# Optimization experiments

Hardware: AMD Instinct MI355X
Metric: run time of the kernel (lower is better)

## Reference

```python
import jax, jax.numpy as jnp
import numpy as np

N_HEADS = 16
PROJ_DIM = 64  # per-head dim
DIM = N_HEADS * PROJ_DIM  # 1024


def setup_inputs() -> dict:
    key = jax.random.key(0)
    k1, k2, k3, k4, k5 = jax.random.split(key, 5)
    N, L = 2, 2048
    scale = 1.0 / np.sqrt(DIM)
    return {
        "query": jax.random.normal(k1, (N, L, DIM), dtype=jnp.float32),
        "key": jax.random.normal(k2, (N, L, DIM), dtype=jnp.float32),
        "Wq": jax.random.normal(k3, (DIM, DIM), dtype=jnp.float32) * scale,
        "Wk": jax.random.normal(k4, (DIM, DIM), dtype=jnp.float32) * scale,
        "Wv": jax.random.normal(k5, (DIM, DIM), dtype=jnp.float32) * scale,
    }


def reference(query, key, Wq, Wk, Wv):
    # Causal linear-complexity attention (mask=True branch, left_first=False).
    N, Lq, _ = query.shape
    Lk = key.shape[1]
    H, Dh = N_HEADS, PROJ_DIM
    # torch Linear: x @ W.T ; reshape to (N, H, L, Dh)
    q = (query @ Wq.T).reshape(N, Lq, H, Dh).transpose(0, 2, 1, 3)
    k = (key @ Wk.T).reshape(N, Lk, H, Dh).transpose(0, 2, 1, 3)
    v = (key @ Wv.T).reshape(N, Lk, H, Dh).transpose(0, 2, 1, 3)
    q = jax.nn.softmax(q, axis=-1)
    k = jax.nn.softmax(k, axis=-1)
    # right[t] = sum_{s<=t} k_s^T v_s  : (N,H,Lk,Dh,Dh) cumulative outer products
    S = jnp.cumsum(jnp.einsum('nhti,nhtj->nhtij', k, v), axis=2)
    out = jnp.einsum('nhti,nhtij->nhtj', q, S)  # (N,H,Lq,Dh)
    return out.transpose(0, 2, 1, 3).reshape(N, Lq, H * Dh)
```

## Files before the change

kernel.cpp:

```cpp
#include <hip/hip_runtime.h>


constexpr int DIM  = 1024;
constexpr int H    = 16;
constexpr int DH   = 64;
constexpr int LSEQ = 2048;
constexpr int NB   = 2;
constexpr int MTOK = NB * LSEQ;
constexpr int CS   = 64;
constexpr int NC   = LSEQ / CS;

typedef __bf16 bf16x8 __attribute__((ext_vector_type(8)));
typedef float floatx4 __attribute__((ext_vector_type(4)));
typedef unsigned short ushort_t;

__device__ __forceinline__ ushort_t f2bf(float f) {
  unsigned int u = __float_as_uint(f);
  u += 0x7FFFu + ((u >> 16) & 1u);
  return (ushort_t)(u >> 16);
}
__device__ __forceinline__ float bf2f(ushort_t b) {
  return __uint_as_float(((unsigned int)b) << 16);
}

__device__ __forceinline__ void async16(void* lds, const void* g) {
  __builtin_amdgcn_global_load_lds(
      (const __attribute__((address_space(1))) unsigned int*)g,
      (__attribute__((address_space(3))) unsigned int*)lds, 16, 0, 0);
}

__device__ __forceinline__ bf16x8 tfrag(const unsigned int* T, int row, int uoff) {
  union { bf16x8 v; unsigned int u[4]; } r;
  const unsigned int* p = T + row * 33 + uoff;
  r.u[0] = p[0]; r.u[1] = p[1]; r.u[2] = p[2]; r.u[3] = p[3];
  return r.v;
}

__device__ __forceinline__ void transpose_tile(const ushort_t* g, unsigned int* TT, int tid) {
  const int ic = tid & 7, tp = tid >> 3;
  const ushort_t* r0 = g + (size_t)(2 * tp) * DIM + ic * 8;
  union { uint4 q; ushort_t u[8]; } a0, a1;
  a0.q = *(const uint4*)r0;
  a1.q = *(const uint4*)(r0 + DIM);
#pragma unroll
  for (int j = 0; j < 8; j++)
    TT[(8 * ic + j) * 33 + tp] = (unsigned int)a0.u[j] | ((unsigned int)a1.u[j] << 16);
}

__global__ __launch_bounds__(256) void cast_all(const float* __restrict__ q,
                                                const float* __restrict__ k,
                                                const float* __restrict__ wq,
                                                const float* __restrict__ wk,
                                                const float* __restrict__ wv,
                                                ushort_t* __restrict__ xbf,
                                                ushort_t* __restrict__ wbf) {
  const int seg = blockIdx.y;
  const float* src;
  ushort_t* dst;
  int n4;
  if (seg == 0)      { src = q;  dst = xbf;                  n4 = (4 << 20) / 4; }
  else if (seg == 1) { src = k;  dst = xbf + (4 << 20);      n4 = (4 << 20) / 4; }
  else if (seg == 2) { src = wq; dst = wbf;                  n4 = (1 << 20) / 4; }
  else if (seg == 3) { src = wk; dst = wbf + (1 << 20);      n4 = (1 << 20) / 4; }
  else               { src = wv; dst = wbf + (2 << 20);      n4 = (1 << 20) / 4; }
  for (int i = blockIdx.x * 256 + threadIdx.x; i < n4; i += gridDim.x * 256) {
    const float4 f = ((const float4*)src)[i];
    ((ushort4*)dst)[i] = make_ushort4(f2bf(f.x), f2bf(f.y), f2bf(f.z), f2bf(f.w));
  }
}

struct Stage { ushort_t As[128 * 32]; ushort_t Ws[128 * 32]; };
union SMemU { Stage st[3]; ushort_t CsB[128 * 136]; };

__global__ __launch_bounds__(256) void gemm_fused(const ushort_t* __restrict__ xbf,
                                                  const ushort_t* __restrict__ wbf,
                                                  ushort_t* __restrict__ qp,
                                                  ushort_t* __restrict__ kp,
                                                  ushort_t* __restrict__ vp) {
  __shared__ SMemU sm;
  const int tid  = threadIdx.x;
  const int z    = blockIdx.z;
  const ushort_t* A = xbf + (z ? (size_t)(4 << 20) : 0);
  const ushort_t* W = wbf + (size_t)z * (1 << 20);
  ushort_t* C = (z == 0) ? qp : ((z == 1) ? kp : vp);
  const int bn   = blockIdx.x * 128;
  const int bm   = blockIdx.y * 128;
  const int lane = tid & 63;
  const int wid  = tid >> 6;
  const int wm   = wid >> 1, wn = wid & 1;
  const int row16 = lane & 15, quad = lane >> 4;

  floatx4 acc[4][4] = {};

  const int srow = tid >> 2;
  const int cg   = (tid & 3) ^ ((srow ^ (srow >> 2)) & 3);
  const ushort_t* gA0 = A + (size_t)(bm + srow) * DIM + cg * 8;
  const ushort_t* gA1 = A + (size_t)(bm + 64 + srow) * DIM + cg * 8;
  const ushort_t* gW0 = W + (size_t)(bn + srow) * DIM + cg * 8;
  const ushort_t* gW1 = W + (size_t)(bn + 64 + srow) * DIM + cg * 8;

#define STAGE(buf, koff)                                    \
  {                                                         \
    Stage& s_ = sm.st[buf];                                 \
    async16(s_.As + tid * 8,         gA0 + (koff));         \
    async16(s_.As + (tid + 256) * 8, gA1 + (koff));         \
    async16(s_.Ws + tid * 8,         gW0 + (koff));         \
    async16(s_.Ws + (tid + 256) * 8, gW1 + (koff));         \
  }

  const int qx   = quad ^ ((row16 ^ (row16 >> 2)) & 3);
  const int aoff = (wm * 64 + row16) * 32 + qx * 8;
  const int boff = (wn * 64 + row16) * 32 + qx * 8;

  STAGE(0, 0);
  STAGE(1, 32);

  int cur = 0, pf = 2;
  for (int s = 0; s < 32; ++s) {
    if (s < 31) asm volatile("s_waitcnt vmcnt(4)" ::: "memory");
    else        asm volatile("s_waitcnt vmcnt(0)" ::: "memory");
    __builtin_amdgcn_s_barrier();
    if (s + 2 < 32) STAGE(pf, (s + 2) * 32);

    const Stage& st = sm.st[cur];
    bf16x8 a[4], b[4];
#pragma unroll
    for (int mt = 0; mt < 4; mt++)
      a[mt] = *(const bf16x8*)&st.As[aoff + mt * 512];
#pragma unroll
    for (int nt = 0; nt < 4; nt++)
      b[nt] = *(const bf16x8*)&st.Ws[boff + nt * 512];
#pragma unroll
    for (int mt = 0; mt < 4; mt++)
#pragma unroll
      for (int nt = 0; nt < 4; nt++)
        acc[mt][nt] = __builtin_amdgcn_mfma_f32_16x16x32_bf16(a[mt], b[nt], acc[mt][nt], 0, 0, 0);

    cur = (cur == 2) ? 0 : cur + 1;
    pf  = (pf  == 2) ? 0 : pf + 1;
  }
#undef STAGE
  __syncthreads();

  if (z < 2) {
#pragma unroll
    for (int mt = 0; mt < 4; mt++)
#pragma unroll
      for (int r = 0; r < 4; r++) {
        float m = fmaxf(fmaxf(acc[mt][0][r], acc[mt][1][r]),
                        fmaxf(acc[mt][2][r], acc[mt][3][r]));
#pragma unroll
        for (int o = 1; o < 16; o <<= 1) m = fmaxf(m, __shfl_xor(m, o, 64));
        float e[4], s = 0.f;
#pragma unroll
        for (int nt = 0; nt < 4; nt++) { e[nt] = __expf(acc[mt][nt][r] - m); s += e[nt]; }
#pragma unroll
        for (int o = 1; o < 16; o <<= 1) s += __shfl_xor(s, o, 64);
        const float inv = 1.f / s;
#pragma unroll
        for (int nt = 0; nt < 4; nt++) acc[mt][nt][r] = e[nt] * inv;
      }
  }

#pragma unroll
  for (int mt = 0; mt < 4; mt++)
#pragma unroll
    for (int nt = 0; nt < 4; nt++)
#pragma unroll
      for (int r = 0; r < 4; r++)
        sm.CsB[(wm * 64 + mt * 16 + quad * 4 + r) * 136 + wn * 64 + nt * 16 + row16] =
            f2bf(acc[mt][nt][r]);
  __syncthreads();
#pragma unroll
  for (int it = 0; it < 8; it++) {
    const int ch = tid + it * 256;
    const int row = ch >> 4, ic = ch & 15;
    const uint4 val = *(const uint4*)&sm.CsB[row * 136 + ic * 8];
    *(uint4*)&C[(size_t)(bm + row) * DIM + bn + ic * 8] = val;
  }
}

__global__ __launch_bounds__(256) void chunk_T(const ushort_t* __restrict__ kp,
                                               const ushort_t* __restrict__ vp,
                                               float* __restrict__ cs) {
  __shared__ unsigned int KT[64 * 33];
  __shared__ unsigned int VT[64 * 33];
  const int c = blockIdx.x, h = blockIdx.y, n = blockIdx.z;
  const int tid = threadIdx.x;
  const size_t gbase = ((size_t)(n * LSEQ + c * CS)) * DIM + h * DH;

  transpose_tile(kp + gbase, KT, tid);
  transpose_tile(vp + gbase, VT, tid);
  __syncthreads();

  const int lane = tid & 63, wid = tid >> 6;
  const int row16 = lane & 15, quad = lane >> 4;

  floatx4 acc[4] = {};
#pragma unroll
  for (int ks = 0; ks < 2; ks++) {
    const bf16x8 a = tfrag(VT, wid * 16 + row16, ks * 16 + quad * 4);
#pragma unroll
    for (int nt = 0; nt < 4; nt++) {
      const bf16x8 b = tfrag(KT, nt * 16 + row16, ks * 16 + quad * 4);
      acc[nt] = __builtin_amdgcn_mfma_f32_16x16x32_bf16(a, b, acc[nt], 0, 0, 0);
    }
  }
  float* outp = cs + ((size_t)((n * H + h) * NC + c)) * (DH * DH);
#pragma unroll
  for (int nt = 0; nt < 4; nt++)
#pragma unroll
    for (int r = 0; r < 4; r++)
      outp[(wid * 16 + quad * 4 + r) * DH + nt * 16 + row16] = acc[nt][r];
}

__global__ __launch_bounds__(256) void prefix_chunks(const float* __restrict__ cs,
                                                     ushort_t* __restrict__ csb) {
  const int nh = blockIdx.x >> 4;
  const int e  = (blockIdx.x & 15) * 256 + threadIdx.x;
  const float* bf_ = cs + (size_t)nh * NC * (DH * DH) + e;
  ushort_t* bb = csb + (size_t)nh * NC * (DH * DH) + e;
  float run = 0.f;
#pragma unroll
  for (int c = 0; c < NC; c++) {
    const float cur = bf_[(size_t)c * (DH * DH)];
    bb[(size_t)c * (DH * DH)] = f2bf(run);
    run += cur;
  }
}

__global__ __launch_bounds__(256) void attn_mfma(const ushort_t* __restrict__ qp,
                                                 const ushort_t* __restrict__ kp,
                                                 const ushort_t* __restrict__ vp,
                                                 const ushort_t* __restrict__ csb,
                                                 float* __restrict__ out) {
  __shared__ ushort_t Qs[64 * 72];
  __shared__ ushort_t Ks[64 * 72];
  __shared__ ushort_t Ts[64 * 72];
  __shared__ unsigned int VT[64 * 33];
  __shared__ ushort_t Pb[64 * 72];
  const int c = blockIdx.x, h = blockIdx.y, n = blockIdx.z;
  const int tid = threadIdx.x;
  const size_t gbase = ((size_t)(n * LSEQ + c * CS)) * DIM + h * DH;
  const size_t cbase = ((size_t)((n * H + h) * NC + c)) * (DH * DH);

#pragma unroll
  for (int it = 0; it < 2; it++) {
    const int ch = tid + it * 256;
    const int row = ch >> 3, ic = ch & 7;
    *(uint4*)&Qs[row * 72 + ic * 8] = *(const uint4*)&qp[gbase + (size_t)row * DIM + ic * 8];
    *(uint4*)&Ks[row * 72 + ic * 8] = *(const uint4*)&kp[gbase + (size_t)row * DIM + ic * 8];
    *(uint4*)&Ts[row * 72 + ic * 8] = *(const uint4*)&csb[cbase + (size_t)row * DH + ic * 8];
  }
  transpose_tile(vp + gbase, VT, tid);
  __syncthreads();

  const int lane = tid & 63, wid = tid >> 6;
  const int row16 = lane & 15, quad = lane >> 4;
  const int t0 = wid * 16;

  floatx4 acc[4] = {};
  floatx4 pacc[4] = {};

#pragma unroll
  for (int ks = 0; ks < 2; ks++) {
    const bf16x8 aq = *(const bf16x8*)&Qs[(t0 + row16) * 72 + ks * 32 + quad * 8];
#pragma unroll
    for (int nt = 0; nt < 4; nt++) {
      const bf16x8 bt = *(const bf16x8*)&Ts[(nt * 16 + row16) * 72 + ks * 32 + quad * 8];
      acc[nt] = __builtin_amdgcn_mfma_f32_16x16x32_bf16(aq, bt, acc[nt], 0, 0, 0);
      const bf16x8 bk = *(const bf16x8*)&Ks[(nt * 16 + row16) * 72 + ks * 32 + quad * 8];
      pacc[nt] = __builtin_amdgcn_mfma_f32_16x16x32_bf16(aq, bk, pacc[nt], 0, 0, 0);
    }
  }
#pragma unroll
  for (int nt = 0; nt < 4; nt++)
#pragma unroll
    for (int r = 0; r < 4; r++) {
      const int t = t0 + quad * 4 + r, s = nt * 16 + row16;
      Pb[t * 72 + s] = f2bf((s <= t) ? pacc[nt][r] : 0.f);
    }
  __syncthreads();

#pragma unroll
  for (int ks = 0; ks < 2; ks++) {
    const bf16x8 ap = *(const bf16x8*)&Pb[(t0 + row16) * 72 + ks * 32 + quad * 8];
#pragma unroll
    for (int nt = 0; nt < 4; nt++) {
      const bf16x8 bv = tfrag(VT, nt * 16 + row16, ks * 16 + quad * 4);
      acc[nt] = __builtin_amdgcn_mfma_f32_16x16x32_bf16(ap, bv, acc[nt], 0, 0, 0);
    }
  }

#pragma unroll
  for (int nt = 0; nt < 4; nt++)
#pragma unroll
    for (int r = 0; r < 4; r++)
      out[gbase + (size_t)(t0 + quad * 4 + r) * DIM + nt * 16 + row16] = acc[nt][r];
}

extern "C" void kernel_launch(void* const* d_in, const int* in_sizes, int n_in,
                              void* d_out, int out_size, void* d_ws, size_t ws_size,
                              hipStream_t stream) {
  const float* query = (const float*)d_in[0];
  const float* key   = (const float*)d_in[1];
  const float* Wq    = (const float*)d_in[2];
  const float* Wk    = (const float*)d_in[3];
  const float* Wv    = (const float*)d_in[4];
  float* out = (float*)d_out;

  const size_t PM = (size_t)4 << 20;
  ushort_t* qp = (ushort_t*)d_ws;
  ushort_t* kp = qp + PM;
  ushort_t* vp = kp + PM;
  float*    cs = (float*)(vp + PM);
  ushort_t* csb = (ushort_t*)(cs + PM);
  ushort_t* xbf = (ushort_t*)cs;
  ushort_t* wbf = (ushort_t*)out;

  cast_all<<<dim3(512, 5), 256, 0, stream>>>(query, key, Wq, Wk, Wv, xbf, wbf);

  gemm_fused<<<dim3(DIM / 128, MTOK / 128, 3), 256, 0, stream>>>(xbf, wbf, qp, kp, vp);

  chunk_T<<<dim3(NC, H, NB), 256, 0, stream>>>(kp, vp, cs);
  prefix_chunks<<<dim3(NB * H * 16), 256, 0, stream>>>(cs, csb);
  attn_mfma<<<dim3(NC, H, NB), 256, 0, stream>>>(qp, kp, vp, csb, out);
}
```

Baseline: 158.2 us.

## Fuse chunk, prefix and attention stages into persistent kernel with grid barriers

Replaces the three tail launches (per-chunk KᵀV, chunk prefix sum, per-chunk attention) with one persistent 768-block kernel. Each block handles one or two tiles, and the stages are separated by a software grid barrier built on global atomics. Separately, the projection GEMM moves to a flat 1D grid with an XCD-aware remap, so blocks sharing the same A rows land on the same XCD's L2. This removes launch gaps and improves cache locality. It depends on all 768 blocks being co-resident; if they are not, the spin barrier can deadlock.

```diff
diff --git a/kernel.cpp b/kernel.cpp
--- a/kernel.cpp
+++ b/kernel.cpp
@@ -9,6 +9,8 @@
 constexpr int MTOK = NB * LSEQ;
 constexpr int CS   = 64;
 constexpr int NC   = LSEQ / CS;
+constexpr int NTILE = NC * H * NB;
+constexpr int TGRID = 768;
 
 typedef __bf16 bf16x8 __attribute__((ext_vector_type(8)));
 typedef float floatx4 __attribute__((ext_vector_type(4)));
@@ -18,9 +20,6 @@
   unsigned int u = __float_as_uint(f);
   u += 0x7FFFu + ((u >> 16) & 1u);
   return (ushort_t)(u >> 16);
-}
-__device__ __forceinline__ float bf2f(ushort_t b) {
-  return __uint_as_float(((unsigned int)b) << 16);
 }
 
 __device__ __forceinline__ void async16(void* lds, const void* g) {
@@ -45,6 +44,27 @@
 #pragma unroll
   for (int j = 0; j < 8; j++)
     TT[(8 * ic + j) * 33 + tp] = (unsigned int)a0.u[j] | ((unsigned int)a1.u[j] << 16);
+}
+
+__device__ int g_bar = 0;
+__device__ int g_gen = 0;
+
+__device__ __forceinline__ void grid_sync_all() {
+  __syncthreads();
+  if (threadIdx.x == 0) {
+    __threadfence();
+    const int g = __hip_atomic_load(&g_gen, __ATOMIC_RELAXED, __HIP_MEMORY_SCOPE_AGENT);
+    if (__hip_atomic_fetch_add(&g_bar, 1, __ATOMIC_ACQ_REL, __HIP_MEMORY_SCOPE_AGENT)
+        == TGRID - 1) {
+      __hip_atomic_store(&g_bar, 0, __ATOMIC_RELAXED, __HIP_MEMORY_SCOPE_AGENT);
+      __hip_atomic_fetch_add(&g_gen, 1, __ATOMIC_RELEASE, __HIP_MEMORY_SCOPE_AGENT);
+    } else {
+      while (__hip_atomic_load(&g_gen, __ATOMIC_ACQUIRE, __HIP_MEMORY_SCOPE_AGENT) == g)
+        __builtin_amdgcn_s_sleep(1);
+    }
+    __threadfence();
+  }
+  __syncthreads();
 }
 
 __global__ __launch_bounds__(256) void cast_all(const float* __restrict__ q,
@@ -79,12 +99,18 @@
                                                   ushort_t* __restrict__ vp) {
   __shared__ SMemU sm;
   const int tid  = threadIdx.x;
-  const int z    = blockIdx.z;
+
+  const int flat  = blockIdx.x;
+  const int xcd   = flat & 7;
+  const int local = flat >> 3;
+  const int z     = local >> 5;
+  const int l2    = local & 31;
+  const int bn    = (l2 & 7) * 128;
+  const int bm    = (xcd * 4 + (l2 >> 3)) * 128;
+
   const ushort_t* A = xbf + (z ? (size_t)(4 << 20) : 0);
   const ushort_t* W = wbf + (size_t)z * (1 << 20);
   ushort_t* C = (z == 0) ? qp : ((z == 1) ? kp : vp);
-  const int bn   = blockIdx.x * 128;
-  const int bm   = blockIdx.y * 128;
   const int lane = tid & 63;
   const int wid  = tid >> 6;
   const int wm   = wid >> 1, wn = wid & 1;
@@ -180,123 +206,130 @@
   }
 }
 
-__global__ __launch_bounds__(256) void chunk_T(const ushort_t* __restrict__ kp,
-                                               const ushort_t* __restrict__ vp,
-                                               float* __restrict__ cs) {
-  __shared__ unsigned int KT[64 * 33];
+__global__ __launch_bounds__(256, 3) void fused_tail(const ushort_t* __restrict__ qp,
+                                                     const ushort_t* __restrict__ kp,
+                                                     const ushort_t* __restrict__ vp,
+                                                     float* __restrict__ cs,
+                                                     ushort_t* __restrict__ csb,
+                                                     float* __restrict__ out) {
   __shared__ unsigned int VT[64 * 33];
-  const int c = blockIdx.x, h = blockIdx.y, n = blockIdx.z;
+  __shared__ union TailU {
+    unsigned int KT[64 * 33];
+    struct { ushort_t Qs[64 * 72]; ushort_t Ks[64 * 72];
+             ushort_t Ts[64 * 72]; ushort_t Pb[64 * 72]; } p3;
+  } u;
+
+  const int blk = blockIdx.x;
   const int tid = threadIdx.x;
-  const size_t gbase = ((size_t)(n * LSEQ + c * CS)) * DIM + h * DH;
-
-  transpose_tile(kp + gbase, KT, tid);
-  transpose_tile(vp + gbase, VT, tid);
-  __syncthreads();
-
   const int lane = tid & 63, wid = tid >> 6;
   const int row16 = lane & 15, quad = lane >> 4;
 
-  floatx4 acc[4] = {};
-#pragma unroll
-  for (int ks = 0; ks < 2; ks++) {
-    const bf16x8 a = tfrag(VT, wid * 16 + row16, ks * 16 + quad * 4);
-#pragma unroll
-    for (int nt = 0; nt < 4; nt++) {
-      const bf16x8 b = tfrag(KT, nt * 16 + row16, ks * 16 + quad * 4);
-      acc[nt] = __builtin_amdgcn_mfma_f32_16x16x32_bf16(a, b, acc[nt], 0, 0, 0);
-    }
-  }
-  float* outp = cs + ((size_t)((n * H + h) * NC + c)) * (DH * DH);
-#pragma unroll
-  for (int nt = 0; nt < 4; nt++)
-#pragma unroll
-    for (int r = 0; r < 4; r++)
-      outp[(wid * 16 + quad * 4 + r) * DH + nt * 16 + row16] = acc[nt][r];
-}
-
-__global__ __launch_bounds__(256) void prefix_chunks(const float* __restrict__ cs,
-                                                     ushort_t* __restrict__ csb) {
-  const int nh = blockIdx.x >> 4;
-  const int e  = (blockIdx.x & 15) * 256 + threadIdx.x;
-  const float* bf_ = cs + (size_t)nh * NC * (DH * DH) + e;
-  ushort_t* bb = csb + (size_t)nh * NC * (DH * DH) + e;
-  float run = 0.f;
-#pragma unroll
-  for (int c = 0; c < NC; c++) {
-    const float cur = bf_[(size_t)c * (DH * DH)];
-    bb[(size_t)c * (DH * DH)] = f2bf(run);
-    run += cur;
-  }
-}
-
-__global__ __launch_bounds__(256) void attn_mfma(const ushort_t* __restrict__ qp,
-                                                 const ushort_t* __restrict__ kp,
-                                                 const ushort_t* __restrict__ vp,
-                                                 const ushort_t* __restrict__ csb,
-                                                 float* __restrict__ out) {
-  __shared__ ushort_t Qs[64 * 72];
-  __shared__ ushort_t Ks[64 * 72];
-  __shared__ ushort_t Ts[64 * 72];
-  __shared__ unsigned int VT[64 * 33];
-  __shared__ ushort_t Pb[64 * 72];
-  const int c = blockIdx.x, h = blockIdx.y, n = blockIdx.z;
-  const int tid = threadIdx.x;
-  const size_t gbase = ((size_t)(n * LSEQ + c * CS)) * DIM + h * DH;
-  const size_t cbase = ((size_t)((n * H + h) * NC + c)) * (DH * DH);
-
-#pragma unroll
-  for (int it = 0; it < 2; it++) {
-    const int ch = tid + it * 256;
-    const int row = ch >> 3, ic = ch & 7;
-    *(uint4*)&Qs[row * 72 + ic * 8] = *(const uint4*)&qp[gbase + (size_t)row * DIM + ic * 8];
-    *(uint4*)&Ks[row * 72 + ic * 8] = *(const uint4*)&kp[gbase + (size_t)row * DIM + ic * 8];
-    *(uint4*)&Ts[row * 72 + ic * 8] = *(const uint4*)&csb[cbase + (size_t)row * DH + ic * 8];
-  }
-  transpose_tile(vp + gbase, VT, tid);
-  __syncthreads();
-
-  const int lane = tid & 63, wid = tid >> 6;
-  const int row16 = lane & 15, quad = lane >> 4;
-  const int t0 = wid * 16;
-
-  floatx4 acc[4] = {};
-  floatx4 pacc[4] = {};
-
-#pragma unroll
-  for (int ks = 0; ks < 2; ks++) {
-    const bf16x8 aq = *(const bf16x8*)&Qs[(t0 + row16) * 72 + ks * 32 + quad * 8];
-#pragma unroll
-    for (int nt = 0; nt < 4; nt++) {
-      const bf16x8 bt = *(const bf16x8*)&Ts[(nt * 16 + row16) * 72 + ks * 32 + quad * 8];
-      acc[nt] = __builtin_amdgcn_mfma_f32_16x16x32_bf16(aq, bt, acc[nt], 0, 0, 0);
-      const bf16x8 bk = *(const bf16x8*)&Ks[(nt * 16 + row16) * 72 + ks * 32 + quad * 8];
-      pacc[nt] = __builtin_amdgcn_mfma_f32_16x16x32_bf16(aq, bk, pacc[nt], 0, 0, 0);
-    }
-  }
-#pragma unroll
-  for (int nt = 0; nt < 4; nt++)
-#pragma unroll
-    for (int r = 0; r < 4; r++) {
-      const int t = t0 + quad * 4 + r, s = nt * 16 + row16;
-      Pb[t * 72 + s] = f2bf((s <= t) ? pacc[nt][r] : 0.f);
-    }
-  __syncthreads();
-
-#pragma unroll
-  for (int ks = 0; ks < 2; ks++) {
-    const bf16x8 ap = *(const bf16x8*)&Pb[(t0 + row16) * 72 + ks * 32 + quad * 8];
-#pragma unroll
-    for (int nt = 0; nt < 4; nt++) {
-      const bf16x8 bv = tfrag(VT, nt * 16 + row16, ks * 16 + quad * 4);
-      acc[nt] = __builtin_amdgcn_mfma_f32_16x16x32_bf16(ap, bv, acc[nt], 0, 0, 0);
-    }
-  }
-
-#pragma unroll
-  for (int nt = 0; nt < 4; nt++)
-#pragma unroll
-    for (int r = 0; r < 4; r++)
-      out[gbase + (size_t)(t0 + quad * 4 + r) * DIM + nt * 16 + row16] = acc[nt][r];
+  int tiles[2];
+  int ntiles = 0;
+  tiles[ntiles++] = blk;
+  if (blk + TGRID < NTILE) tiles[ntiles++] = blk + TGRID;
+
+  for (int i = 0; i < ntiles; i++) {
+    const int t = tiles[i];
+    const int c = t & 31, h = (t >> 5) & 15, n = t >> 9;
+    const size_t gbase = ((size_t)(n * LSEQ + c * CS)) * DIM + h * DH;
+    if (i) __syncthreads();
+    transpose_tile(kp + gbase, u.KT, tid);
+    transpose_tile(vp + gbase, VT, tid);
+    __syncthreads();
+
+    floatx4 acc[4] = {};
+#pragma unroll
+    for (int ks = 0; ks < 2; ks++) {
+      const bf16x8 a = tfrag(VT, wid * 16 + row16, ks * 16 + quad * 4);
+#pragma unroll
+      for (int nt = 0; nt < 4; nt++) {
+        const bf16x8 b = tfrag(u.KT, nt * 16 + row16, ks * 16 + quad * 4);
+        acc[nt] = __builtin_amdgcn_mfma_f32_16x16x32_bf16(a, b, acc[nt], 0, 0, 0);
+      }
+    }
+    float* outp = cs + ((size_t)((n * H + h) * NC + c)) * (DH * DH);
+#pragma unroll
+    for (int nt = 0; nt < 4; nt++)
+#pragma unroll
+      for (int r = 0; r < 4; r++)
+        outp[(wid * 16 + quad * 4 + r) * DH + nt * 16 + row16] = acc[nt][r];
+  }
+  grid_sync_all();
+
+  if (blk < NB * H * 16) {
+    const int nh = blk >> 4;
+    const int e  = (blk & 15) * 256 + tid;
+    const float* bf_ = cs + (size_t)nh * NC * (DH * DH) + e;
+    ushort_t* bb = csb + (size_t)nh * NC * (DH * DH) + e;
+    float run = 0.f;
+#pragma unroll
+    for (int c = 0; c < NC; c++) {
+      const float cur = bf_[(size_t)c * (DH * DH)];
+      bb[(size_t)c * (DH * DH)] = f2bf(run);
+      run += cur;
+    }
+  }
+  grid_sync_all();
+
+  for (int i = 0; i < ntiles; i++) {
+    const int t = tiles[i];
+    const int c = t & 31, h = (t >> 5) & 15, n = t >> 9;
+    const size_t gbase = ((size_t)(n * LSEQ + c * CS)) * DIM + h * DH;
+    const size_t cbase = ((size_t)((n * H + h) * NC + c)) * (DH * DH);
+    __syncthreads();
+
+#pragma unroll
+    for (int it = 0; it < 2; it++) {
+      const int ch = tid + it * 256;
+      const int row = ch >> 3, ic = ch & 7;
+      *(uint4*)&u.p3.Qs[row * 72 + ic * 8] = *(const uint4*)&qp[gbase + (size_t)row * DIM + ic * 8];
+      *(uint4*)&u.p3.Ks[row * 72 + ic * 8] = *(const uint4*)&kp[gbase + (size_t)row * DIM + ic * 8];
+      *(uint4*)&u.p3.Ts[row * 72 + ic * 8] = *(const uint4*)&csb[cbase + (size_t)row * DH + ic * 8];
+    }
+    transpose_tile(vp + gbase, VT, tid);
+    __syncthreads();
+
+    const int t0 = wid * 16;
+    floatx4 acc[4] = {};
+    floatx4 pacc[4] = {};
+
+#pragma unroll
+    for (int ks = 0; ks < 2; ks++) {
+      const bf16x8 aq = *(const bf16x8*)&u.p3.Qs[(t0 + row16) * 72 + ks * 32 + quad * 8];
+#pragma unroll
+      for (int nt = 0; nt < 4; nt++) {
+        const bf16x8 bt = *(const bf16x8*)&u.p3.Ts[(nt * 16 + row16) * 72 + ks * 32 + quad * 8];
+        acc[nt] = __builtin_amdgcn_mfma_f32_16x16x32_bf16(aq, bt, acc[nt], 0, 0, 0);
+        const bf16x8 bk = *(const bf16x8*)&u.p3.Ks[(nt * 16 + row16) * 72 + ks * 32 + quad * 8];
+        pacc[nt] = __builtin_amdgcn_mfma_f32_16x16x32_bf16(aq, bk, pacc[nt], 0, 0, 0);
+      }
+    }
+#pragma unroll
+    for (int nt = 0; nt < 4; nt++)
+#pragma unroll
+      for (int r = 0; r < 4; r++) {
+        const int tt = t0 + quad * 4 + r, ss = nt * 16 + row16;
+        u.p3.Pb[tt * 72 + ss] = f2bf((ss <= tt) ? pacc[nt][r] : 0.f);
+      }
+    __syncthreads();
+
+#pragma unroll
+    for (int ks = 0; ks < 2; ks++) {
+      const bf16x8 ap = *(const bf16x8*)&u.p3.Pb[(t0 + row16) * 72 + ks * 32 + quad * 8];
+#pragma unroll
+      for (int nt = 0; nt < 4; nt++) {
+        const bf16x8 bv = tfrag(VT, nt * 16 + row16, ks * 16 + quad * 4);
+        acc[nt] = __builtin_amdgcn_mfma_f32_16x16x32_bf16(ap, bv, acc[nt], 0, 0, 0);
+      }
+    }
+
+#pragma unroll
+    for (int nt = 0; nt < 4; nt++)
+#pragma unroll
+      for (int r = 0; r < 4; r++)
+        out[gbase + (size_t)(t0 + quad * 4 + r) * DIM + nt * 16 + row16] = acc[nt][r];
+  }
 }
 
 extern "C" void kernel_launch(void* const* d_in, const int* in_sizes, int n_in,
@@ -320,9 +353,7 @@
 
   cast_all<<<dim3(512, 5), 256, 0, stream>>>(query, key, Wq, Wk, Wv, xbf, wbf);
 
-  gemm_fused<<<dim3(DIM / 128, MTOK / 128, 3), 256, 0, stream>>>(xbf, wbf, qp, kp, vp);
-
-  chunk_T<<<dim3(NC, H, NB), 256, 0, stream>>>(kp, vp, cs);
-  prefix_chunks<<<dim3(NB * H * 16), 256, 0, stream>>>(cs, csb);
-  attn_mfma<<<dim3(NC, H, NB), 256, 0, stream>>>(qp, kp, vp, csb, out);
-}
+  gemm_fused<<<dim3(768), 256, 0, stream>>>(xbf, wbf, qp, kp, vp);
+
+  fused_tail<<<dim3(TGRID), 256, 0, stream>>>(qp, kp, vp, cs, csb, out);
+}
```

Result: slower. 419.1 us (+164.8%).
